# Kernel optimization log

Hardware: AMD Instinct MI355X
Metric: run time of the kernel (lower is better)

## Reference

```python
import jax, jax.numpy as jnp
import numpy as np
from jax import lax

EPS = 1e-5


def _bn_eval(x, gamma, beta, mean, var, axis=1):
    # eval-mode batchnorm over channel axis
    shape = [1] * x.ndim
    shape[axis] = -1
    g = gamma.reshape(shape); b = beta.reshape(shape)
    m = mean.reshape(shape); v = var.reshape(shape)
    return (x - m) * (g * lax.rsqrt(v + EPS)) + b


def setup_inputs() -> dict:
    key = jax.random.key(0)
    ks = jax.random.split(key, 12)
    B, C, H, W, K = 16, 256, 128, 128, 5
    x_feat = jax.random.normal(ks[0], (B, C, H, W), jnp.float32)
    raw_img = jax.random.uniform(ks[1], (B, 3, H, W), jnp.float32)
    # img_feature: Conv2d(3,64,3,pad=1) + BN(64)
    w_conv1 = jax.random.normal(ks[2], (64, 3, 3, 3), jnp.float32) * 0.1
    b_conv1 = jax.random.normal(ks[3], (64,), jnp.float32) * 0.1
    g1 = jnp.ones((64,), jnp.float32)
    beta1 = jnp.zeros((64,), jnp.float32)
    m1 = jax.random.normal(ks[4], (64,), jnp.float32) * 0.1
    v1 = jax.random.uniform(ks[5], (64,), jnp.float32) + 0.5
    # conv_filter: Conv2d(64, C*K*K, 1) + BN(C*K*K)
    CK2 = C * K * K
    w_filt = jax.random.normal(ks[6], (CK2, 64), jnp.float32) * 0.05
    b_filt = jax.random.normal(ks[7], (CK2,), jnp.float32) * 0.05
    g2 = jnp.ones((CK2,), jnp.float32)
    beta2 = jnp.zeros((CK2,), jnp.float32)
    m2 = jax.random.normal(ks[8], (CK2,), jnp.float32) * 0.1
    v2 = jax.random.uniform(ks[9], (CK2,), jnp.float32) + 0.5
    return {"x_feat": x_feat, "raw_img": raw_img,
            "w_conv1": w_conv1, "b_conv1": b_conv1, "g1": g1, "beta1": beta1, "m1": m1, "v1": v1,
            "w_filt": w_filt, "b_filt": b_filt, "g2": g2, "beta2": beta2, "m2": m2, "v2": v2}


def reference(x_feat, raw_img, w_conv1, b_conv1, g1, beta1, m1, v1,
              w_filt, b_filt, g2, beta2, m2, v2):
    B, C, H, W = x_feat.shape
    K = int(round(np.sqrt(w_filt.shape[0] // C)))  # kernel_size
    pad = K // 2

    # ---- filter generation branch ----
    # Conv2d(3,64,3,pad=1)
    y = lax.conv_general_dilated(raw_img, w_conv1, (1, 1), ((1, 1), (1, 1)),
                                 dimension_numbers=("NCHW", "OIHW", "NCHW"))
    y = y + b_conv1[None, :, None, None]
    y = jax.nn.relu(_bn_eval(y, g1, beta1, m1, v1))
    img_feat = jnp.mean(y, axis=(2, 3))                        # (B, 64) global avg pool

    # 1x1 conv == dense: (B, C*K*K)
    df = img_feat @ w_filt.T + b_filt
    df = _bn_eval(df[:, :, None, None], g2, beta2, m2, v2)[:, :, 0, 0]
    df = df.reshape(B, C, K * K)
    # NOTE: original applies Softmax(dim=1) -> over the CHANNEL axis
    df = jax.nn.softmax(df, axis=1)                            # (B, C, K*K)

    # ---- per-sample dynamic depthwise conv ----
    x_pad = jnp.pad(x_feat, ((0, 0), (0, 0), (pad, pad), (pad, pad)), mode="reflect")
    filt = df.reshape(B, C, K, K)

    def dw(x, w):  # x: (C, Hp, Wp), w: (C, K, K)
        return lax.conv_general_dilated(
            x[None], w[:, None], (1, 1), "VALID",
            dimension_numbers=("NCHW", "OIHW", "NCHW"),
            feature_group_count=C)[0]

    out = jax.vmap(dw)(x_pad, filt)                            # (B, C, H, W)
    return out
```

## Files before the change

### kernel.cpp

```cpp
#include <hip/hip_runtime.h>

#define EPSV 1e-5f

typedef float f4 __attribute__((ext_vector_type(4)));
typedef float f2 __attribute__((ext_vector_type(2)));

#define B   16
#define CIN 3
#define C1  64
#define C   256
#define H   128
#define W   128
#define K   5
#define KK  25
#define FSTR 28

#define R1  8
#define CH1 (H / R1)
#define TW1 132

__global__ __launch_bounds__(256) void k1_conv_pool(
    const float* __restrict__ raw, const float* __restrict__ wconv,
    const float* __restrict__ bconv, const float* __restrict__ g1,
    const float* __restrict__ be1, const float* __restrict__ m1,
    const float* __restrict__ v1, float* __restrict__ partial)
{
  const int b     = blockIdx.x >> 4;
  const int chunk = blockIdx.x & 15;
  const int tid   = threadIdx.x;

  __shared__ __align__(16) float tile[CIN][R1 + 2][TW1];
  const float* rawb = raw + (size_t)b * CIN * H * W;
  for (int i = tid; i < CIN * (R1 + 2) * TW1; i += 256) {
    int ic  = i / ((R1 + 2) * TW1);
    int rem = i - ic * (R1 + 2) * TW1;
    int r   = rem / TW1;
    int cc  = rem - r * TW1;
    int gr  = chunk * R1 + r - 1;
    int gc  = cc - 1;
    float val = 0.f;
    if ((unsigned)gr < H && (unsigned)gc < W)
      val = rawb[ic * H * W + gr * W + gc];
    tile[ic][r][cc] = val;
  }
  __syncthreads();

  const int row = tid >> 5;
  const int grp = tid & 31;
  float wt[2][27], bias[2], sc[2], mn[2], bt[2];
#pragma unroll
  for (int g = 0; g < 2; ++g) {
    int c = grp * 2 + g;
#pragma unroll
    for (int k = 0; k < 27; ++k) wt[g][k] = wconv[c * 27 + k];
    bias[g] = bconv[c];
    sc[g]   = g1[c] * rsqrtf(v1[c] + EPSV);
    mn[g]   = m1[c];
    bt[g]   = be1[c];
  }

  float acc0 = 0.f, acc1 = 0.f;
  for (int w = 0; w < W; w += 4) {
    float v[2][4];
#pragma unroll
    for (int p = 0; p < 4; ++p) { v[0][p] = bias[0]; v[1][p] = bias[1]; }
#pragma unroll
    for (int ic = 0; ic < CIN; ++ic) {
#pragma unroll
      for (int kh = 0; kh < 3; ++kh) {
        f4 a  = *(const f4*)&tile[ic][row + kh][w];
        f4 bb = *(const f4*)&tile[ic][row + kh][w + 4];
#pragma unroll
        for (int p = 0; p < 4; ++p) {
#pragma unroll
          for (int kw = 0; kw < 3; ++kw) {
            float e = (p + kw < 4) ? a[p + kw] : bb[p + kw - 4];
            v[0][p] += e * wt[0][ic * 9 + kh * 3 + kw];
            v[1][p] += e * wt[1][ic * 9 + kh * 3 + kw];
          }
        }
      }
    }
#pragma unroll
    for (int p = 0; p < 4; ++p) {
      acc0 += fmaxf((v[0][p] - mn[0]) * sc[0] + bt[0], 0.f);
      acc1 += fmaxf((v[1][p] - mn[1]) * sc[1] + bt[1], 0.f);
    }
  }

  __shared__ float red[R1][C1];
  red[row][grp * 2]     = acc0;
  red[row][grp * 2 + 1] = acc1;
  __syncthreads();
  if (tid < C1) {
    float s = 0.f;
#pragma unroll
    for (int r = 0; r < R1; ++r) s += red[r][tid];
    partial[((size_t)b * CH1 + chunk) * C1 + tid] = s;
  }
}

__global__ __launch_bounds__(256) void k2_filter(
    const float* __restrict__ partial, const float* __restrict__ wf,
    const float* __restrict__ bf, const float* __restrict__ g2,
    const float* __restrict__ be2, const float* __restrict__ m2,
    const float* __restrict__ v2, float* __restrict__ filt)
{
  const int b  = blockIdx.x / KK;
  const int kk = blockIdx.x - b * KK;
  const int c  = threadIdx.x;

  __shared__ float feat[C1];
  if (c < C1) {
    float s = 0.f;
#pragma unroll
    for (int ch = 0; ch < CH1; ++ch)
      s += partial[((size_t)b * CH1 + ch) * C1 + c];
    feat[c] = s * (1.f / (H * W));
  }
  __syncthreads();

  const int idx = c * KK + kk;
  float v = bf[idx];
  const float* wr = wf + (size_t)idx * C1;
#pragma unroll
  for (int j = 0; j < C1; ++j) v += feat[j] * wr[j];
  v = (v - m2[idx]) * (g2[idx] * rsqrtf(v2[idx] + EPSV)) + be2[idx];

  __shared__ float red[256];
  red[c] = v;
  __syncthreads();
#pragma unroll
  for (int s = 128; s > 0; s >>= 1) {
    if (c < s) red[c] = fmaxf(red[c], red[c + s]);
    __syncthreads();
  }
  float mx = red[0];
  __syncthreads();
  float e = expf(v - mx);
  red[c] = e;
  __syncthreads();
#pragma unroll
  for (int s = 128; s > 0; s >>= 1) {
    if (c < s) red[c] += red[c + s];
    __syncthreads();
  }
  filt[((size_t)b * C + c) * FSTR + kk] = e / red[0];
}

#define R3  32
#define TW3 132
#define TH3 (R3 + 4)

__global__ __launch_bounds__(512) void k3_dwconv(
    const float* __restrict__ x, const float* __restrict__ filt,
    float* __restrict__ out)
{
  const int bid = blockIdx.x;
  const int swz = (bid & 7) * 2048 + (bid >> 3);
  const int plane = swz >> 2;
  const int tile  = swz & 3;
  const int r0    = tile * R3;
  const int tid   = threadIdx.x;

  const float* xp = x + (size_t)plane * H * W;
  float* op       = out + (size_t)plane * H * W;
  const float* fp = filt + (size_t)plane * FSTR;

  f4 fv[7];
#pragma unroll
  for (int i = 0; i < 7; ++i) fv[i] = *(const f4*)&fp[i << 2];

  __shared__ __align__(16) float t[TH3][TW3];

  for (int idx = tid; idx < TH3 * 32; idx += 512) {
    int r = idx >> 5, g = idx & 31;
    int gr = r0 + r - 2;
    gr = gr < 0 ? -gr : (gr >= H ? 2 * H - 2 - gr : gr);
    f4 v = *(const f4*)&xp[gr * W + (g << 2)];
    f2 lo = {v[0], v[1]};
    f2 hi = {v[2], v[3]};
    *(f2*)&t[r][(g << 2) + 2] = lo;
    *(f2*)&t[r][(g << 2) + 4] = hi;
  }
  if (tid < TH3 * 4) {
    int r = tid >> 2, c = tid & 3;
    int cc = (c == 0) ? 0 : (c == 1) ? 1 : (c == 2) ? 130 : 131;
    int gc = (c == 0) ? 2 : (c == 1) ? 1 : (c == 2) ? 126 : 125;
    int gr = r0 + r - 2;
    gr = gr < 0 ? -gr : (gr >= H ? 2 * H - 2 - gr : gr);
    t[r][cc] = xp[gr * W + gc];
  }
  __syncthreads();

  const int g  = tid & 31, w = g << 2;
  const int rb = (tid >> 5) << 1;
  f4 acc0 = {0.f, 0.f, 0.f, 0.f};
  f4 acc1 = {0.f, 0.f, 0.f, 0.f};
#pragma unroll
  for (int i = 0; i < 6; ++i) {
    f4 a  = *(const f4*)&t[rb + i][w];
    f4 bb = *(const f4*)&t[rb + i][w + 4];
#pragma unroll
    for (int p = 0; p < 4; ++p) {
#pragma unroll
      for (int j = 0; j < 5; ++j) {
        float e = (p + j < 4) ? a[p + j] : bb[p + j - 4];
        if (i <= 4) {
          const int k0 = i * 5 + j;
          acc0[p] += e * fv[k0 >> 2][k0 & 3];
        }
        if (i >= 1) {
          const int k1 = (i - 1) * 5 + j;
          acc1[p] += e * fv[k1 >> 2][k1 & 3];
        }
      }
    }
  }
  __builtin_nontemporal_store(acc0, (f4*)&op[(r0 + rb) * W + w]);
  __builtin_nontemporal_store(acc1, (f4*)&op[(r0 + rb + 1) * W + w]);
}

extern "C" void kernel_launch(void* const* d_in, const int* in_sizes, int n_in,
                              void* d_out, int out_size, void* d_ws, size_t ws_size,
                              hipStream_t stream) {
  const float* x_feat = (const float*)d_in[0];
  const float* raw    = (const float*)d_in[1];
  const float* wconv  = (const float*)d_in[2];
  const float* bconv  = (const float*)d_in[3];
  const float* g1     = (const float*)d_in[4];
  const float* be1    = (const float*)d_in[5];
  const float* m1     = (const float*)d_in[6];
  const float* v1     = (const float*)d_in[7];
  const float* wf     = (const float*)d_in[8];
  const float* bf     = (const float*)d_in[9];
  const float* g2     = (const float*)d_in[10];
  const float* be2    = (const float*)d_in[11];
  const float* m2     = (const float*)d_in[12];
  const float* v2     = (const float*)d_in[13];
  float* out = (float*)d_out;

  float* partial = (float*)d_ws;
  float* filt    = partial + B * CH1 * C1;

  k1_conv_pool<<<B * CH1, 256, 0, stream>>>(raw, wconv, bconv, g1, be1, m1, v1, partial);
  k2_filter  <<<B * KK, 256, 0, stream>>>(partial, wf, bf, g2, be2, m2, v2, filt);
  k3_dwconv  <<<B * C * (H / R3), 512, 0, stream>>>(x_feat, filt, out);
}
```

Baseline: 138.8 us.

## Split conv1 across width tiles with register sliding window; enlarge dwconv row tiles

The first conv kernel now splits each row chunk into four width slices, giving 1024 blocks of 128 threads instead of 256 blocks. Each thread computes two output rows using a register-held sliding window of input vectors, and the batchnorm is folded into a single multiply-add. The filter kernel now sums 64 partials per sample to match. The depthwise conv doubles its row tile to 64 rows and has each thread compute 4 output rows, reusing each loaded shared-memory row across up to 4 accumulators. This cuts LDS traffic and halo overhead, at the cost of more registers and fewer blocks for the dominant kernel.

```diff
diff --git a/kernel.cpp b/kernel.cpp
--- a/kernel.cpp
+++ b/kernel.cpp
@@ -15,90 +15,117 @@
 #define KK  25
 #define FSTR 28
 
-#define R1  8
-#define CH1 (H / R1)
-#define TW1 132
-
-__global__ __launch_bounds__(256) void k1_conv_pool(
+#define R1   8
+#define WS1  32
+#define TW1  36
+
+__global__ __launch_bounds__(128) void k1_conv_pool(
     const float* __restrict__ raw, const float* __restrict__ wconv,
     const float* __restrict__ bconv, const float* __restrict__ g1,
     const float* __restrict__ be1, const float* __restrict__ m1,
     const float* __restrict__ v1, float* __restrict__ partial)
 {
-  const int b     = blockIdx.x >> 4;
-  const int chunk = blockIdx.x & 15;
+  const int bid   = blockIdx.x;
+  const int b     = bid >> 6;
+  const int chunk = (bid >> 2) & 15;
+  const int wh    = bid & 3;
   const int tid   = threadIdx.x;
 
-  __shared__ __align__(16) float tile[CIN][R1 + 2][TW1];
+  __shared__ __align__(16) float t[CIN][R1 + 2][TW1];
   const float* rawb = raw + (size_t)b * CIN * H * W;
-  for (int i = tid; i < CIN * (R1 + 2) * TW1; i += 256) {
-    int ic  = i / ((R1 + 2) * TW1);
-    int rem = i - ic * (R1 + 2) * TW1;
-    int r   = rem / TW1;
-    int cc  = rem - r * TW1;
+  for (int i = tid; i < CIN * (R1 + 2) * 34; i += 128) {
+    int ic  = i / ((R1 + 2) * 34);
+    int rem = i - ic * (R1 + 2) * 34;
+    int r   = rem / 34;
+    int cc  = rem - r * 34;
     int gr  = chunk * R1 + r - 1;
-    int gc  = cc - 1;
+    int gc  = wh * WS1 + cc - 1;
     float val = 0.f;
     if ((unsigned)gr < H && (unsigned)gc < W)
       val = rawb[ic * H * W + gr * W + gc];
-    tile[ic][r][cc] = val;
-  }
-  __syncthreads();
-
-  const int row = tid >> 5;
+    t[ic][r][cc] = val;
+  }
+  __syncthreads();
+
+  const int rp  = tid >> 5;
   const int grp = tid & 31;
-  float wt[2][27], bias[2], sc[2], mn[2], bt[2];
+  float wt[2][27], A[2], Bc[2];
 #pragma unroll
   for (int g = 0; g < 2; ++g) {
     int c = grp * 2 + g;
 #pragma unroll
     for (int k = 0; k < 27; ++k) wt[g][k] = wconv[c * 27 + k];
-    bias[g] = bconv[c];
-    sc[g]   = g1[c] * rsqrtf(v1[c] + EPSV);
-    mn[g]   = m1[c];
-    bt[g]   = be1[c];
-  }
+    float sc = g1[c] * rsqrtf(v1[c] + EPSV);
+    A[g]  = sc;
+    Bc[g] = (bconv[c] - m1[c]) * sc + be1[c];
+  }
+
+  f4 cur[CIN][4], nxt[CIN][4];
+#pragma unroll
+  for (int ic = 0; ic < CIN; ++ic)
+#pragma unroll
+    for (int r = 0; r < 4; ++r) cur[ic][r] = *(const f4*)&t[ic][2 * rp + r][0];
 
   float acc0 = 0.f, acc1 = 0.f;
-  for (int w = 0; w < W; w += 4) {
-    float v[2][4];
-#pragma unroll
-    for (int p = 0; p < 4; ++p) { v[0][p] = bias[0]; v[1][p] = bias[1]; }
+#pragma unroll
+  for (int j = 0; j < 8; ++j) {
+#pragma unroll
+    for (int ic = 0; ic < CIN; ++ic)
+#pragma unroll
+      for (int r = 0; r < 4; ++r) nxt[ic][r] = *(const f4*)&t[ic][2 * rp + r][4 * j + 4];
+
+    float v[2][2][4];
+#pragma unroll
+    for (int q = 0; q < 2; ++q)
+#pragma unroll
+      for (int g = 0; g < 2; ++g)
+#pragma unroll
+        for (int p = 0; p < 4; ++p) v[q][g][p] = 0.f;
+
 #pragma unroll
     for (int ic = 0; ic < CIN; ++ic) {
 #pragma unroll
-      for (int kh = 0; kh < 3; ++kh) {
-        f4 a  = *(const f4*)&tile[ic][row + kh][w];
-        f4 bb = *(const f4*)&tile[ic][row + kh][w + 4];
-#pragma unroll
-        for (int p = 0; p < 4; ++p) {
-#pragma unroll
-          for (int kw = 0; kw < 3; ++kw) {
-            float e = (p + kw < 4) ? a[p + kw] : bb[p + kw - 4];
-            v[0][p] += e * wt[0][ic * 9 + kh * 3 + kw];
-            v[1][p] += e * wt[1][ic * 9 + kh * 3 + kw];
+      for (int q = 0; q < 2; ++q) {
+#pragma unroll
+        for (int kh = 0; kh < 3; ++kh) {
+          f4 a  = cur[ic][q + kh];
+          f4 bb = nxt[ic][q + kh];
+#pragma unroll
+          for (int p = 0; p < 4; ++p) {
+#pragma unroll
+            for (int kw = 0; kw < 3; ++kw) {
+              float e = (p + kw < 4) ? a[p + kw] : bb[p + kw - 4];
+              v[q][0][p] += e * wt[0][ic * 9 + kh * 3 + kw];
+              v[q][1][p] += e * wt[1][ic * 9 + kh * 3 + kw];
+            }
           }
         }
       }
     }
 #pragma unroll
-    for (int p = 0; p < 4; ++p) {
-      acc0 += fmaxf((v[0][p] - mn[0]) * sc[0] + bt[0], 0.f);
-      acc1 += fmaxf((v[1][p] - mn[1]) * sc[1] + bt[1], 0.f);
-    }
-  }
-
-  __shared__ float red[R1][C1];
-  red[row][grp * 2]     = acc0;
-  red[row][grp * 2 + 1] = acc1;
+    for (int q = 0; q < 2; ++q)
+#pragma unroll
+      for (int p = 0; p < 4; ++p) {
+        acc0 += fmaxf(v[q][0][p] * A[0] + Bc[0], 0.f);
+        acc1 += fmaxf(v[q][1][p] * A[1] + Bc[1], 0.f);
+      }
+#pragma unroll
+    for (int ic = 0; ic < CIN; ++ic)
+#pragma unroll
+      for (int r = 0; r < 4; ++r) cur[ic][r] = nxt[ic][r];
+  }
+
+  __shared__ float red[4][C1];
+  red[rp][grp * 2]     = acc0;
+  red[rp][grp * 2 + 1] = acc1;
   __syncthreads();
   if (tid < C1) {
-    float s = 0.f;
-#pragma unroll
-    for (int r = 0; r < R1; ++r) s += red[r][tid];
-    partial[((size_t)b * CH1 + chunk) * C1 + tid] = s;
-  }
-}
+    float s = red[0][tid] + red[1][tid] + red[2][tid] + red[3][tid];
+    partial[((size_t)((b * 16 + chunk) * 4 + wh)) * C1 + tid] = s;
+  }
+}
+
+#define NCH 64
 
 __global__ __launch_bounds__(256) void k2_filter(
     const float* __restrict__ partial, const float* __restrict__ wf,
@@ -114,8 +141,8 @@
   if (c < C1) {
     float s = 0.f;
 #pragma unroll
-    for (int ch = 0; ch < CH1; ++ch)
-      s += partial[((size_t)b * CH1 + ch) * C1 + c];
+    for (int ch = 0; ch < NCH; ++ch)
+      s += partial[((size_t)b * NCH + ch) * C1 + c];
     feat[c] = s * (1.f / (H * W));
   }
   __syncthreads();
@@ -148,7 +175,7 @@
   filt[((size_t)b * C + c) * FSTR + kk] = e / red[0];
 }
 
-#define R3  32
+#define R3  64
 #define TW3 132
 #define TH3 (R3 + 4)
 
@@ -157,9 +184,9 @@
     float* __restrict__ out)
 {
   const int bid = blockIdx.x;
-  const int swz = (bid & 7) * 2048 + (bid >> 3);
-  const int plane = swz >> 2;
-  const int tile  = swz & 3;
+  const int swz = (bid & 7) * 1024 + (bid >> 3);
+  const int plane = swz >> 1;
+  const int tile  = swz & 1;
   const int r0    = tile * R3;
   const int tid   = threadIdx.x;
 
@@ -173,6 +200,7 @@
 
   __shared__ __align__(16) float t[TH3][TW3];
 
+#pragma unroll
   for (int idx = tid; idx < TH3 * 32; idx += 512) {
     int r = idx >> 5, g = idx & 31;
     int gr = r0 + r - 2;
@@ -194,31 +222,33 @@
   __syncthreads();
 
   const int g  = tid & 31, w = g << 2;
-  const int rb = (tid >> 5) << 1;
-  f4 acc0 = {0.f, 0.f, 0.f, 0.f};
-  f4 acc1 = {0.f, 0.f, 0.f, 0.f};
-#pragma unroll
-  for (int i = 0; i < 6; ++i) {
-    f4 a  = *(const f4*)&t[rb + i][w];
-    f4 bb = *(const f4*)&t[rb + i][w + 4];
-#pragma unroll
-    for (int p = 0; p < 4; ++p) {
-#pragma unroll
-      for (int j = 0; j < 5; ++j) {
-        float e = (p + j < 4) ? a[p + j] : bb[p + j - 4];
-        if (i <= 4) {
-          const int k0 = i * 5 + j;
-          acc0[p] += e * fv[k0 >> 2][k0 & 3];
-        }
-        if (i >= 1) {
-          const int k1 = (i - 1) * 5 + j;
-          acc1[p] += e * fv[k1 >> 2][k1 & 3];
+  const int rb = (tid >> 5) << 2;
+  f4 acc[4];
+#pragma unroll
+  for (int q = 0; q < 4; ++q) acc[q] = (f4){0.f, 0.f, 0.f, 0.f};
+
+#pragma unroll
+  for (int tr = 0; tr < 8; ++tr) {
+    f4 a  = *(const f4*)&t[rb + tr][w];
+    f4 bb = *(const f4*)&t[rb + tr][w + 4];
+#pragma unroll
+    for (int q = 0; q < 4; ++q) {
+      if (tr - q < 0 || tr - q > 4) continue;
+      const int ki = tr - q;
+#pragma unroll
+      for (int p = 0; p < 4; ++p) {
+#pragma unroll
+        for (int j = 0; j < 5; ++j) {
+          float e = (p + j < 4) ? a[p + j] : bb[p + j - 4];
+          const int k = ki * 5 + j;
+          acc[q][p] += e * fv[k >> 2][k & 3];
         }
       }
     }
   }
-  __builtin_nontemporal_store(acc0, (f4*)&op[(r0 + rb) * W + w]);
-  __builtin_nontemporal_store(acc1, (f4*)&op[(r0 + rb + 1) * W + w]);
+#pragma unroll
+  for (int q = 0; q < 4; ++q)
+    __builtin_nontemporal_store(acc[q], (f4*)&op[(r0 + rb + q) * W + w]);
 }
 
 extern "C" void kernel_launch(void* const* d_in, const int* in_sizes, int n_in,
@@ -241,9 +271,9 @@
   float* out = (float*)d_out;
 
   float* partial = (float*)d_ws;
-  float* filt    = partial + B * CH1 * C1;
-
-  k1_conv_pool<<<B * CH1, 256, 0, stream>>>(raw, wconv, bconv, g1, be1, m1, v1, partial);
+  float* filt    = partial + B * NCH * C1;
+
+  k1_conv_pool<<<B * 16 * 4, 128, 0, stream>>>(raw, wconv, bconv, g1, be1, m1, v1, partial);
   k2_filter  <<<B * KK, 256, 0, stream>>>(partial, wf, bf, g2, be2, m2, v2, filt);
   k3_dwconv  <<<B * C * (H / R3), 512, 0, stream>>>(x_feat, filt, out);
 }
```

Result: faster. 128.8 us (-7.2%).
